# Optimization experiments

Hardware: AMD Instinct MI355X
Metric: run time of the kernel (lower is better)

Reference implementation:

```python
import jax, jax.numpy as jnp
import numpy as np

ALPHA = 0.2
NEG = -9e15


def gat_layer(h, adj, W, a):
    # h: [B,N,Fin], adj: [B,N,N], W: [Fin,Fout], a: [2*Fout,1]
    Wh = jnp.matmul(h, W)                       # [B,N,Fout]
    Fout = W.shape[1]
    a1 = a[:Fout, 0]                             # source part
    a2 = a[Fout:, 0]                             # target part
    # e_ij = LeakyReLU(a1.Wh_i + a2.Wh_j) -- avoids O(N^2*2F) concat
    e = jax.nn.leaky_relu(
        (Wh @ a1)[:, :, None] + (Wh @ a2)[:, None, :], negative_slope=ALPHA
    )                                            # [B,N,N]
    att = jax.nn.softmax(jnp.where(adj > 0, e, NEG), axis=2)
    return jnp.matmul(att, Wh)                  # [B,N,Fout]


def setup_inputs() -> dict:
    key = jax.random.key(0)
    ks = jax.random.split(key, 6)
    B, N, F_IN, F_HID, F_OUT, H = 16, 1024, 256, 64, 64, 4
    x = jax.random.normal(ks[0], (B, N, F_IN), dtype=jnp.float32)
    adj = jax.random.randint(ks[1], (B, N, N), 0, 2, dtype=jnp.int32)
    W_heads = jax.random.normal(ks[2], (H, F_IN, F_HID), dtype=jnp.float32) * 0.1
    a_heads = jax.random.normal(ks[3], (H, 2 * F_HID, 1), dtype=jnp.float32) * 0.1
    W_out = jax.random.normal(ks[4], (H * F_HID, F_OUT), dtype=jnp.float32) * 0.1
    a_out = jax.random.normal(ks[5], (2 * F_OUT, 1), dtype=jnp.float32) * 0.1
    return {"x": x, "adj": adj, "W_heads": W_heads, "a_heads": a_heads,
            "W_out": W_out, "a_out": a_out}


def reference(x, adj, W_heads, a_heads, W_out, a_out):
    # multi-head: vmap over heads -> [H,B,N,F_hid]
    heads = jax.vmap(lambda W, a: gat_layer(x, adj, W, a))(W_heads, a_heads)
    H, B, N, Fh = heads.shape
    h_cat = jnp.transpose(heads, (1, 2, 0, 3)).reshape(B, N, H * Fh)
    out = jax.nn.elu(gat_layer(h_cat, adj, W_out, a_out))  # [B,N,nclass]
    return jnp.mean(out, axis=1)                           # [B,nclass]
```

## Files before the change

kernel.cpp:

```cpp
#include <hip/hip_runtime.h>
#include <math.h>

#define BB 16
#define NN 1024
#define FH 64
#define NH 4
#define LOG2E 1.4426950408889634f

typedef __attribute__((ext_vector_type(8))) short short8;
typedef __attribute__((ext_vector_type(4))) float f32x4;
typedef __attribute__((ext_vector_type(4))) unsigned u32x4;
typedef unsigned long long u64;
typedef unsigned short ushort_t;

__device__ inline unsigned f2bf(float x) {
    unsigned u = __builtin_bit_cast(unsigned, x);
    u += 0x7fff + ((u >> 16) & 1);
    return u >> 16;
}
__device__ inline unsigned pkbf(float lo, float hi) {
    unsigned r;
    asm("v_cvt_pk_bf16_f32 %0, %1, %2" : "=v"(r) : "v"(lo), "v"(hi));
    return r;
}

__global__ void pack_kernel(const int* __restrict__ adj, u64* __restrict__ bm,
                            const float* __restrict__ Whd, const float* __restrict__ Wo,
                            ushort_t* __restrict__ BT1, ushort_t* __restrict__ BT2) {
    const int row = blockIdx.x * 4 + (threadIdx.x >> 6);
    const int lane = threadIdx.x & 63;
    const int* __restrict__ ar = adj + (size_t)row * NN;
    #pragma unroll
    for (int g = 0; g < 16; ++g) {
        u64 m = __ballot(ar[g * 64 + lane] > 0);
        if (lane == 0) bm[row * 16 + g] = m;
    }
    const int col = blockIdx.x, k = threadIdx.x;
    if (col < 256)      BT1[col * 256 + k] = (ushort_t)f2bf(Whd[(col >> 6) * 16384 + k * 64 + (col & 63)]);
    else if (col < 320) BT2[(col - 256) * 256 + k] = (ushort_t)f2bf(Wo[k * 64 + (col - 256)]);
}

template <int A_BF16>
__global__ __launch_bounds__(256, 4) void gemm_fused(
    const void* __restrict__ Ap, const ushort_t* __restrict__ BT,
    const float* __restrict__ av, ushort_t* __restrict__ WhbT,
    float* __restrict__ s1, float* __restrict__ s2, const int S) {
    constexpr int K = 256;
    __shared__ __align__(16) short tbuf[64][72];
    const int tid = threadIdx.x;
    const int w = tid >> 6, l = tid & 63, lo = l & 15, kg = l >> 4;

    const int nx = gridDim.x;
    const int id = blockIdx.y * nx + blockIdx.x;
    const int nwg = nx * gridDim.y;
    const int lid = (id & 7) * (nwg >> 3) + (id >> 3);
    const int row0 = (lid / nx) * 64, col0 = (lid % nx) * 64;

    const int b = row0 >> 10, j0 = row0 & (NN - 1);
    const int hsel = col0 >> 6;

    f32x4 acc[4];
    #pragma unroll
    for (int cb = 0; cb < 4; ++cb) acc[cb] = (f32x4){0.f, 0.f, 0.f, 0.f};

    if (A_BF16) {
        const ushort_t* __restrict__ arow = (const ushort_t*)Ap + (size_t)(row0 + w * 16 + lo) * K;
        #pragma unroll
        for (int ks = 0; ks < 8; ++ks) {
            const int k0 = ks * 32 + kg * 8;
            const short8 af = *(const short8*)(arow + k0);
            #pragma unroll
            for (int cb = 0; cb < 4; ++cb) {
                const short8 bf = *(const short8*)(BT + (size_t)(col0 + cb * 16 + lo) * K + k0);
                acc[cb] = __builtin_amdgcn_mfma_f32_16x16x32_bf16(af, bf, acc[cb], 0, 0, 0);
            }
        }
    } else {
        const float* __restrict__ arow = (const float*)Ap + (size_t)(row0 + w * 16 + lo) * K;
        #pragma unroll
        for (int ks = 0; ks < 8; ++ks) {
            const int k0 = ks * 32 + kg * 8;
            const float4 a0 = *(const float4*)(arow + k0);
            const float4 a1 = *(const float4*)(arow + k0 + 4);
            u32x4 ap;
            ap[0] = pkbf(a0.x, a0.y); ap[1] = pkbf(a0.z, a0.w);
            ap[2] = pkbf(a1.x, a1.y); ap[3] = pkbf(a1.z, a1.w);
            const short8 af = __builtin_bit_cast(short8, ap);
            #pragma unroll
            for (int cb = 0; cb < 4; ++cb) {
                const short8 bf = *(const short8*)(BT + (size_t)(col0 + cb * 16 + lo) * K + k0);
                acc[cb] = __builtin_amdgcn_mfma_f32_16x16x32_bf16(af, bf, acc[cb], 0, 0, 0);
            }
        }
    }

    float a1v[4], a2v[4];
    #pragma unroll
    for (int cb = 0; cb < 4; ++cb) {
        a1v[cb] = av[hsel * 128 + cb * 16 + lo];
        a2v[cb] = av[hsel * 128 + 64 + cb * 16 + lo];
    }
    float sp1[4], sp2[4];
    #pragma unroll
    for (int r = 0; r < 4; ++r) {
        sp1[r] = acc[0][r] * a1v[0] + acc[1][r] * a1v[1] + acc[2][r] * a1v[2] + acc[3][r] * a1v[3];
        sp2[r] = acc[0][r] * a2v[0] + acc[1][r] * a2v[1] + acc[2][r] * a2v[2] + acc[3][r] * a2v[3];
    }
    #pragma unroll
    for (int m = 1; m < 16; m <<= 1) {
        #pragma unroll
        for (int r = 0; r < 4; ++r) {
            sp1[r] += __shfl_xor(sp1[r], m);
            sp2[r] += __shfl_xor(sp2[r], m);
        }
    }
    if (lo == 0) {
        #pragma unroll
        for (int r = 0; r < 4; ++r) {
            const int R = row0 + w * 16 + kg * 4 + r;
            s1[hsel * (BB * NN) + R] = sp1[r];
            s2[hsel * (BB * NN) + R] = sp2[r] * LOG2E;
        }
    }

    #pragma unroll
    for (int cb = 0; cb < 4; ++cb)
        #pragma unroll
        for (int rp = 0; rp < 2; ++rp)
            ((unsigned*)tbuf)[(cb * 16 + lo) * 36 + w * 8 + kg * 2 + rp] =
                pkbf(acc[cb][rp * 2], acc[cb][rp * 2 + 1]);
    __syncthreads();
    const int fl = tid >> 2, ch = tid & 3;
    const short8 v0 = *(const short8*)((const short*)tbuf + fl * 72 + ch * 16);
    const short8 v1 = *(const short8*)((const short*)tbuf + fl * 72 + ch * 16 + 8);
    ushort_t* dst = WhbT + ((size_t)(b * S) + col0 + fl) * NN + j0 + ch * 16;
    *(short8*)dst = v0;
    *(short8*)(dst + 8) = v1;
}

template <int H, int JQ, int OUT_BF16>
__global__ __launch_bounds__(256, 4) void apply_kernel(
    const ushort_t* __restrict__ WhbT, const int S,
    const float* __restrict__ s1, const float* __restrict__ s2,
    const unsigned* __restrict__ bm32,
    void* __restrict__ outp, float* __restrict__ sums) {
    constexpr int JLEN = NN / JQ;
    constexpr int BW = JLEN / 32;
    constexpr int NCH = JLEN / 64;
    constexpr int SB = 2 * 8192;
    constexpr int UBUF = SB;

    __shared__ __align__(16) float s2s[JLEN];
    __shared__ unsigned bs[64][BW + 1];
    __shared__ __align__(16) char ubuf[UBUF];
    auto stage = (unsigned (*)[64][32])ubuf;

    const int Bk = blockIdx.x;
    const int lid = (Bk & 7) * 128 + (Bk >> 3);
    const int it = lid & 15;
    const int b  = (lid >> 4) & 15;
    const int z  = lid >> 8;
    const int h  = (H > 1) ? z : 0;
    const int jq = (JQ > 1) ? z : 0;
    const int j0g = jq * JLEN;

    const int tid = threadIdx.x;
    const int w = tid >> 6, l = tid & 63;
    const int lo = l & 15, kg = l >> 4;
    const int iloc = w * 16 + lo;
    const int rbase = b * NN + it * 64;
    const int gi = rbase + iloc;
    const int hb = h * (BB * NN);

    const ushort_t* __restrict__ whb = WhbT + ((size_t)(b * S + h * FH)) * NN + j0g;

    const int r0 = tid >> 3, st = tid & 7;
    const int sw = (st ^ (r0 & 7)) * 4;
    const size_t ga = (size_t)r0 * NN + st * 8;
    const size_t gb = (size_t)(r0 + 32) * NN + st * 8;

    int4 cva0 = *(const int4*)(whb + ga);
    int4 cva1 = *(const int4*)(whb + gb);

    const float* __restrict__ s2g = s2 + hb + b * NN + j0g;
    for (int k = tid; k < JLEN / 4; k += 256)
        *(float4*)(s2s + k * 4) = *(const float4*)(s2g + k * 4);
    for (int idx = tid; idx < 64 * BW; idx += 256) {
        int r = idx / BW, wd = idx - r * BW;
        bs[r][wd] = bm32[(size_t)(rbase + r) * 32 + (j0g >> 5) + wd];
    }

    const float s1L = s1[hb + gi] * LOG2E;
    const float Arow = s1L;
    const float Brow = s1L * 0.2f;

    short8 ones;
    #pragma unroll
    for (int e = 0; e < 8; ++e) ones[e] = (short)0x3F80;

    f32x4 acc[4];
    #pragma unroll
    for (int fb = 0; fb < 4; ++fb) acc[fb] = (f32x4){0.f, 0.f, 0.f, 0.f};
    f32x4 accs = (f32x4){0.f, 0.f, 0.f, 0.f};

    *(int4*)&stage[0][r0][sw] = cva0;
    *(int4*)&stage[0][r0 + 32][sw] = cva1;
    if (1 < NCH) {
        cva0 = *(const int4*)(whb + 64 + ga);
        cva1 = *(const int4*)(whb + 64 + gb);
    }
    __syncthreads();

    #pragma unroll
    for (int c = 0; c < NCH; ++c) {
        int4 cvb0, cvb1;
        if (c + 2 < NCH) {
            const ushort_t* src = whb + (c + 2) * 64;
            cvb0 = *(const int4*)(src + ga);
            cvb1 = *(const int4*)(src + gb);
        }
        #pragma unroll
        for (int ks = 0; ks < 2; ++ks) {
            const int kb = c * 64 + ks * 32 + kg * 8;
            const unsigned byte = (bs[iloc][c * 2 + ks] >> (kg * 8)) & 0xFF;
            const float4 sa = *(const float4*)(s2s + kb);
            const float4 sb = *(const float4*)(s2s + kb + 4);
            const float s2r[8] = {sa.x, sa.y, sa.z, sa.w, sb.x, sb.y, sb.z, sb.w};
            float pv[8];
            #pragma unroll
            for (int e = 0; e < 8; ++e) {
                const float t = s2r[e];
                const float u = Arow + t;
                const float v = __builtin_fmaf(t, 0.2f, Brow);
                float ev = fmaxf(u, v);
                ev = ((byte >> e) & 1) ? ev : -1.0e5f;
                pv[e] = __builtin_amdgcn_exp2f(ev);
            }
            u32x4 pk;
            pk[0] = pkbf(pv[0], pv[1]); pk[1] = pkbf(pv[2], pv[3]);
            pk[2] = pkbf(pv[4], pv[5]); pk[3] = pkbf(pv[6], pv[7]);
            const short8 bfr = __builtin_bit_cast(short8, pk);
            __builtin_amdgcn_s_setprio(1);
            #pragma unroll
            for (int fb = 0; fb < 4; ++fb) {
                const int row = fb * 16 + lo;
                const int slot = (ks * 4 + kg) ^ (row & 7);
                const short8 afr = *(const short8*)&stage[c & 1][row][slot * 4];
                acc[fb] = __builtin_amdgcn_mfma_f32_16x16x32_bf16(afr, bfr, acc[fb], 0, 0, 0);
            }
            accs = __builtin_amdgcn_mfma_f32_16x16x32_bf16(ones, bfr, accs, 0, 0, 0);
            __builtin_amdgcn_s_setprio(0);
        }
        if (c + 1 < NCH) {
            *(int4*)&stage[(c + 1) & 1][r0][sw] = cva0;
            *(int4*)&stage[(c + 1) & 1][r0 + 32][sw] = cva1;
        }
        cva0 = cvb0;
        cva1 = cvb1;
        __syncthreads();
    }

    const float inv = OUT_BF16 ? (1.0f / accs[0]) : 1.0f;
    if (!OUT_BF16 && kg == 0)
        sums[(size_t)jq * (BB * NN) + rbase + iloc] = accs[0];

    unsigned* ot = (unsigned*)ubuf;
    #pragma unroll
    for (int fb = 0; fb < 4; ++fb)
        #pragma unroll
        for (int rp = 0; rp < 2; ++rp)
            ot[iloc * 36 + fb * 8 + kg * 2 + rp] =
                pkbf(acc[fb][rp * 2] * inv, acc[fb][rp * 2 + 1] * inv);
    __syncthreads();
    const int i2 = tid >> 2, ch = tid & 3;
    const short8 v0 = *(const short8*)((const short*)ubuf + i2 * 72 + ch * 16);
    const short8 v1 = *(const short8*)((const short*)ubuf + i2 * 72 + ch * 16 + 8);
    if constexpr (OUT_BF16) {
        ushort_t* dst = (ushort_t*)outp + (size_t)(b * NN + it * 64 + i2) * 256 + h * FH + ch * 16;
        *(short8*)dst = v0;
        *(short8*)(dst + 8) = v1;
    } else {
        ushort_t* dst = (ushort_t*)outp + (size_t)jq * (BB * NN * FH)
                      + (size_t)(b * NN + it * 64 + i2) * FH + ch * 16;
        *(short8*)dst = v0;
        *(short8*)(dst + 8) = v1;
    }
}

__global__ __launch_bounds__(256) void mean1_kernel(const ushort_t* __restrict__ part,
                                                    const float* __restrict__ sums,
                                                    float* __restrict__ partial) {
    const int b = blockIdx.x, ck = blockIdx.y;
    const int tid = threadIdx.x;
    const int f = tid & 63, g = tid >> 6;
    float acc = 0.f;
    #pragma unroll
    for (int i = g; i < 64; i += 4) {
        const int row = b * NN + ck * 64 + i;
        const float srow = sums[row] + sums[row + 16384]
                         + sums[row + 32768] + sums[row + 49152];
        float v = 0.f;
        #pragma unroll
        for (int q = 0; q < 4; ++q) {
            const unsigned u = part[(size_t)q * (BB * NN * FH) + (size_t)row * FH + f];
            v += __builtin_bit_cast(float, u << 16);
        }
        v *= (1.0f / srow);
        v = (v > 0.f) ? v : (__builtin_amdgcn_exp2f(v * LOG2E) - 1.0f);
        acc += v;
    }
    __shared__ float r[4][64];
    r[g][f] = acc;
    __syncthreads();
    if (g == 0)
        partial[(b * 16 + ck) * FH + f] = r[0][f] + r[1][f] + r[2][f] + r[3][f];
}

__global__ __launch_bounds__(1024) void mean2_kernel(const float* __restrict__ partial,
                                                     float* __restrict__ out) {
    const int t = threadIdx.x;
    const int b = t >> 6, f = t & 63;
    float s = 0.f;
    #pragma unroll
    for (int ck = 0; ck < 16; ++ck) s += partial[(b * 16 + ck) * FH + f];
    out[b * FH + f] = s * (1.0f / NN);
}

extern "C" void kernel_launch(void* const* d_in, const int* in_sizes, int n_in,
                              void* d_out, int out_size, void* d_ws, size_t ws_size,
                              hipStream_t stream) {
    const float* x       = (const float*)d_in[0];
    const int*   adj     = (const int*)d_in[1];
    const float* W_heads = (const float*)d_in[2];
    const float* a_heads = (const float*)d_in[3];
    const float* W_out   = (const float*)d_in[4];
    const float* a_out   = (const float*)d_in[5];
    float* out = (float*)d_out;
    float* f0  = (float*)d_ws;

    ushort_t* hcat  = (ushort_t*)f0;
    ushort_t* part  = (ushort_t*)f0;
    ushort_t* WhbT1 = (ushort_t*)(f0 + 2097152);
    ushort_t* WhbT2 = (ushort_t*)(f0 + 4194304);
    u64*      bmask = (u64*)(f0 + 4718592);
    ushort_t* WbT1  = (ushort_t*)(f0 + 5242880);
    ushort_t* WbT2  = (ushort_t*)(f0 + 5275648);
    float*    s1_1  = f0 + 5283840;
    float*    s2_1  = s1_1 + 65536;
    float*    s1_2  = s2_1 + 65536;
    float*    s2_2  = s1_2 + 16384;
    float*    sums2 = s2_2 + 16384;
    float*    partial = sums2 + 65536;

    dim3 blk(256);

    pack_kernel<<<dim3(BB * NN / 4), blk, 0, stream>>>(adj, bmask, W_heads, W_out, WbT1, WbT2);

    gemm_fused<0><<<dim3(4, 256), blk, 0, stream>>>(x, WbT1, a_heads, WhbT1, s1_1, s2_1, 256);
    apply_kernel<NH, 1, 1><<<dim3(1024), blk, 0, stream>>>(WhbT1, 256, s1_1, s2_1,
                                                           (const unsigned*)bmask, hcat, nullptr);

    gemm_fused<1><<<dim3(1, 256), blk, 0, stream>>>(hcat, WbT2, a_out, WhbT2, s1_2, s2_2, 64);
    apply_kernel<1, 4, 0><<<dim3(1024), blk, 0, stream>>>(WhbT2, 64, s1_2, s2_2,
                                                          (const unsigned*)bmask, part, sums2);

    mean1_kernel<<<dim3(BB, 16), blk, 0, stream>>>(part, sums2, partial);
    mean2_kernel<<<dim3(1), dim3(1024), 0, stream>>>(partial, out);
}
```

Before: 96.15 us.

## Split second-layer apply over 8 column chunks and fold final mean into atomics

The output-layer attention apply now splits the neighbour dimension into 8 chunks instead of 4 and launches 2048 blocks. The block-index swizzle is generalised to the block count so the larger grid maps correctly. The last reduction kernel is removed: mean1 reduces 8 partials and atomically adds scaled results into the output, which pack_kernel zeroes first. This trades an extra launch for more parallelism on a small grid, at the cost of more partial traffic, float atomics with nondeterministic summation order, and a dependency on workspace sizing for 8 partial buffers.

```diff
diff --git a/kernel.cpp b/kernel.cpp
--- a/kernel.cpp
+++ b/kernel.cpp
@@ -23,10 +23,14 @@
     asm("v_cvt_pk_bf16_f32 %0, %1, %2" : "=v"(r) : "v"(lo), "v"(hi));
     return r;
 }
+__device__ inline float bf2f(short v) {
+    return __builtin_bit_cast(float, (unsigned)((unsigned short)v) << 16);
+}
 
 __global__ void pack_kernel(const int* __restrict__ adj, u64* __restrict__ bm,
                             const float* __restrict__ Whd, const float* __restrict__ Wo,
-                            ushort_t* __restrict__ BT1, ushort_t* __restrict__ BT2) {
+                            ushort_t* __restrict__ BT1, ushort_t* __restrict__ BT2,
+                            float* __restrict__ outz) {
     const int row = blockIdx.x * 4 + (threadIdx.x >> 6);
     const int lane = threadIdx.x & 63;
     const int* __restrict__ ar = adj + (size_t)row * NN;
@@ -38,6 +42,10 @@
     const int col = blockIdx.x, k = threadIdx.x;
     if (col < 256)      BT1[col * 256 + k] = (ushort_t)f2bf(Whd[(col >> 6) * 16384 + k * 64 + (col & 63)]);
     else if (col < 320) BT2[(col - 256) * 256 + k] = (ushort_t)f2bf(Wo[k * 64 + (col - 256)]);
+    if (col == 0) {
+        #pragma unroll
+        for (int i = 0; i < 4; ++i) outz[i * 256 + k] = 0.f;
+    }
 }
 
 template <int A_BF16>
@@ -147,6 +155,7 @@
     constexpr int JLEN = NN / JQ;
     constexpr int BW = JLEN / 32;
     constexpr int NCH = JLEN / 64;
+    constexpr int NB = 16 * 16 * H * JQ;
     constexpr int SB = 2 * 8192;
     constexpr int UBUF = SB;
 
@@ -156,7 +165,7 @@
     auto stage = (unsigned (*)[64][32])ubuf;
 
     const int Bk = blockIdx.x;
-    const int lid = (Bk & 7) * 128 + (Bk >> 3);
+    const int lid = (Bk & 7) * (NB / 8) + (Bk >> 3);
     const int it = lid & 15;
     const int b  = (lid >> 4) & 15;
     const int z  = lid >> 8;
@@ -289,7 +298,7 @@
 
 __global__ __launch_bounds__(256) void mean1_kernel(const ushort_t* __restrict__ part,
                                                     const float* __restrict__ sums,
-                                                    float* __restrict__ partial) {
+                                                    float* __restrict__ out) {
     const int b = blockIdx.x, ck = blockIdx.y;
     const int tid = threadIdx.x;
     const int f = tid & 63, g = tid >> 6;
@@ -297,15 +306,14 @@
     #pragma unroll
     for (int i = g; i < 64; i += 4) {
         const int row = b * NN + ck * 64 + i;
-        const float srow = sums[row] + sums[row + 16384]
-                         + sums[row + 32768] + sums[row + 49152];
+        float s = 0.f;
+        #pragma unroll
+        for (int q = 0; q < 8; ++q) s += sums[(size_t)q * 16384 + row];
         float v = 0.f;
         #pragma unroll
-        for (int q = 0; q < 4; ++q) {
-            const unsigned u = part[(size_t)q * (BB * NN * FH) + (size_t)row * FH + f];
-            v += __builtin_bit_cast(float, u << 16);
-        }
-        v *= (1.0f / srow);
+        for (int q = 0; q < 8; ++q)
+            v += bf2f((short)part[(size_t)q * 1048576 + (size_t)row * FH + f]);
+        v /= s;
         v = (v > 0.f) ? v : (__builtin_amdgcn_exp2f(v * LOG2E) - 1.0f);
         acc += v;
     }
@@ -313,17 +321,8 @@
     r[g][f] = acc;
     __syncthreads();
     if (g == 0)
-        partial[(b * 16 + ck) * FH + f] = r[0][f] + r[1][f] + r[2][f] + r[3][f];
-}
-
-__global__ __launch_bounds__(1024) void mean2_kernel(const float* __restrict__ partial,
-                                                     float* __restrict__ out) {
-    const int t = threadIdx.x;
-    const int b = t >> 6, f = t & 63;
-    float s = 0.f;
-    #pragma unroll
-    for (int ck = 0; ck < 16; ++ck) s += partial[(b * 16 + ck) * FH + f];
-    out[b * FH + f] = s * (1.0f / NN);
+        atomicAdd(&out[b * FH + f],
+                  (r[0][f] + r[1][f] + r[2][f] + r[3][f]) * (1.0f / NN));
 }
 
 extern "C" void kernel_launch(void* const* d_in, const int* in_sizes, int n_in,
@@ -339,7 +338,7 @@
     float* f0  = (float*)d_ws;
 
     ushort_t* hcat  = (ushort_t*)f0;
-    ushort_t* part  = (ushort_t*)f0;
+    ushort_t* part2 = (ushort_t*)f0;
     ushort_t* WhbT1 = (ushort_t*)(f0 + 2097152);
     ushort_t* WhbT2 = (ushort_t*)(f0 + 4194304);
     u64*      bmask = (u64*)(f0 + 4718592);
@@ -350,20 +349,19 @@
     float*    s1_2  = s2_1 + 65536;
     float*    s2_2  = s1_2 + 16384;
     float*    sums2 = s2_2 + 16384;
-    float*    partial = sums2 + 65536;
 
     dim3 blk(256);
 
-    pack_kernel<<<dim3(BB * NN / 4), blk, 0, stream>>>(adj, bmask, W_heads, W_out, WbT1, WbT2);
+    pack_kernel<<<dim3(BB * NN / 4), blk, 0, stream>>>(adj, bmask, W_heads, W_out,
+                                                       WbT1, WbT2, out);
 
     gemm_fused<0><<<dim3(4, 256), blk, 0, stream>>>(x, WbT1, a_heads, WhbT1, s1_1, s2_1, 256);
     apply_kernel<NH, 1, 1><<<dim3(1024), blk, 0, stream>>>(WhbT1, 256, s1_1, s2_1,
                                                            (const unsigned*)bmask, hcat, nullptr);
 
     gemm_fused<1><<<dim3(1, 256), blk, 0, stream>>>(hcat, WbT2, a_out, WhbT2, s1_2, s2_2, 64);
-    apply_kernel<1, 4, 0><<<dim3(1024), blk, 0, stream>>>(WhbT2, 64, s1_2, s2_2,
-                                                          (const unsigned*)bmask, part, sums2);
-
-    mean1_kernel<<<dim3(BB, 16), blk, 0, stream>>>(part, sums2, partial);
-    mean2_kernel<<<dim3(1), dim3(1024), 0, stream>>>(partial, out);
-}
+    apply_kernel<1, 8, 0><<<dim3(2048), blk, 0, stream>>>(WhbT2, 64, s1_2, s2_2,
+                                                          (const unsigned*)bmask, part2, sums2);
+
+    mean1_kernel<<<dim3(BB, 16), blk, 0, stream>>>(part2, sums2, out);
+}
```

Result: slower. 107.0 us (+11.3%).
